# Kernel tuning notes

Hardware: AMD Instinct MI355X
Metric: run time of the kernel (lower is better)

The kernel has to match this reference:

```python
import jax, jax.numpy as jnp
import numpy as np
import math

NH, NKV, HD = 8, 1, 128
SOFTCAP = 30.0
ROPE_BASE = 500000.0


def _rope_tables(T, hd, base):
    half = hd // 2
    inv_freq = 1.0 / (base ** (np.arange(half, dtype=np.float32) / half))
    t = np.arange(T, dtype=np.float32)
    ang = np.outer(t, inv_freq)  # [T, half]
    return jnp.asarray(np.cos(ang)), jnp.asarray(np.sin(ang))


def apply_rope(x, cos, sin):
    # x: [B, T, H, hd]; cos/sin: [T, hd//2]
    half = x.shape[-1] // 2
    x1, x2 = x[..., :half], x[..., half:]
    T = x.shape[1]
    c = cos[:T][None, :, None, :]
    s = sin[:T][None, :, None, :]
    return jnp.concatenate([x1 * c - x2 * s, x1 * s + x2 * c], axis=-1)


def setup_inputs() -> dict:
    key = jax.random.key(0)
    ks = jax.random.split(key, 5)
    B, T, D = 4, 2048, 1024
    KD = NKV * HD
    x = jax.random.normal(ks[0], (B, T, D), dtype=jnp.float32)
    Wq = jax.random.normal(ks[1], (D, D), dtype=jnp.float32) * (D ** -0.5)
    Wk = jax.random.normal(ks[2], (KD, D), dtype=jnp.float32) * (D ** -0.5)
    Wv = jax.random.normal(ks[3], (KD, D), dtype=jnp.float32) * (D ** -0.5)
    Wo = jax.random.normal(ks[4], (D, D), dtype=jnp.float32) * (D ** -0.5)
    qk_gain = jnp.full((NH,), 1.5, dtype=jnp.float32)  # qk_gain_init
    cos, sin = _rope_tables(T, HD, ROPE_BASE)
    return {"x": x, "Wq": Wq, "Wk": Wk, "Wv": Wv, "Wo": Wo,
            "qk_gain": qk_gain, "cos": cos, "sin": sin}


def reference(x, Wq, Wk, Wv, Wo, qk_gain, cos, sin):
    B, T, D = x.shape
    # projections (QuantLinear with qat disabled == plain linear, no bias)
    q = (x @ Wq.T).reshape(B, T, NH, HD)
    k = (x @ Wk.T).reshape(B, T, NKV, HD)
    v = (x @ Wv.T).reshape(B, T, NKV, HD)
    q = apply_rope(q, cos, sin)
    k = apply_rope(k, cos, sin)
    # learned per-head QK gain applied to queries
    q = q * qk_gain[None, None, :, 1 - 1][..., None] if False else q * qk_gain[None, None, :, None]
    # GQA: broadcast the single kv head across NH query heads
    scale = 1.0 / math.sqrt(HD)
    scores = jnp.einsum('bqhd,bkgd->bhqk', q, k) * scale  # g==NKV==1 broadcast
    # logit softcap before masking/softmax
    scores = SOFTCAP * jnp.tanh(scores / SOFTCAP)
    causal = jnp.tril(jnp.ones((T, T), dtype=bool))
    scores = jnp.where(causal[None, None], scores, -jnp.inf)
    attn = jax.nn.softmax(scores, axis=-1)  # [B, NH, T, T]
    out = jnp.einsum('bhqk,bkgd->bqhd', attn, v).reshape(B, T, NH * HD)
    return out @ Wo.T
```

## Files before the change

### kernel.cpp

```cpp
#include <hip/hip_runtime.h>
#include <hip/hip_bf16.h>

#define B_ 4
#define T_ 2048
#define D_ 1024
#define NH_ 8
#define HD_ 128

typedef short short8 __attribute__((ext_vector_type(8)));
typedef float floatx4 __attribute__((ext_vector_type(4)));

#if __has_builtin(__builtin_amdgcn_exp2f)
#define EXP2F __builtin_amdgcn_exp2f
#else
#define EXP2F exp2f
#endif
#if __has_builtin(__builtin_amdgcn_rcpf)
#define RCPF __builtin_amdgcn_rcpf
#else
__device__ __forceinline__ float RCPF(float x) { return 1.f / x; }
#endif

#if __has_builtin(__builtin_amdgcn_global_load_lds)
#define G2L(gp, lp)                                                        \
  __builtin_amdgcn_global_load_lds(                                        \
      (const __attribute__((address_space(1))) unsigned int*)(gp),         \
      (__attribute__((address_space(3))) unsigned int*)(lp), 16, 0, 0)
#else
#define G2L(gp, lp) (*(uint4*)(lp) = *(const uint4*)(gp))
#endif

__device__ __forceinline__ unsigned short f2b(float f) {
  union { float fl; unsigned int i; } v; v.fl = f;
  unsigned int r = v.i + 0x7fffu + ((v.i >> 16) & 1u);
  return (unsigned short)(r >> 16);
}
__device__ __forceinline__ unsigned int pack_bf16(float a, float b) {
  unsigned int ua = __float_as_uint(a) + 0x8000u;
  unsigned int ub = __float_as_uint(b) + 0x8000u;
  return (ua >> 16) | (ub & 0xffff0000u);
}
__device__ __forceinline__ float blo(unsigned int u) { return __uint_as_float(u << 16); }
__device__ __forceinline__ float bhi(unsigned int u) { return __uint_as_float(u & 0xffff0000u); }

__global__ __launch_bounds__(256) void cvt_kernel(
    const float* __restrict__ x,  const float* __restrict__ wq,
    const float* __restrict__ wk, const float* __restrict__ wv,
    const float* __restrict__ wo, unsigned short* __restrict__ dst)
{
  size_t i = ((size_t)blockIdx.x * 256 + threadIdx.x) * 8;
  const float* src; size_t off;
  if      (i <  8388608u) { src = x;  off = i; }
  else if (i <  9437184u) { src = wq; off = i - 8388608u; }
  else if (i <  9568256u) { src = wk; off = i - 9437184u; }
  else if (i <  9699328u) { src = wv; off = i - 9568256u; }
  else                    { src = wo; off = i - 9699328u; }
  float4 a = *(const float4*)(src + off);
  float4 b = *(const float4*)(src + off + 4);
  uint4 o;
  o.x = pack_bf16(a.x, a.y); o.y = pack_bf16(a.z, a.w);
  o.z = pack_bf16(b.x, b.y); o.w = pack_bf16(b.z, b.w);
  *(uint4*)(dst + i) = o;
}

template <bool C_F32>
__device__ __forceinline__ void gemm_body_1024(
    const unsigned short* __restrict__ Arow0,
    const unsigned short* __restrict__ Btile,
    void* __restrict__ Cb, int ldC)
{
  __shared__ unsigned short As[128 * 32];
  __shared__ unsigned short Bs[128 * 32];
  const int tid = threadIdx.x;
  const int lane = tid & 63;
  const int w = tid >> 6;
  const int wr = w >> 1, wc = w & 1;
  const int l15 = lane & 15, quad = lane >> 4;

  const unsigned short* a_src = Arow0 + (size_t)(tid >> 2) * 1024 + (tid & 3) * 8;
  const unsigned short* b_src = Btile + (size_t)(tid >> 2) * 1024 + (tid & 3) * 8;
  unsigned short* a_dst = &As[(tid >> 2) * 32 + (tid & 3) * 8];
  unsigned short* b_dst = &Bs[(tid >> 2) * 32 + (tid & 3) * 8];

  floatx4 zero = {0.f, 0.f, 0.f, 0.f};
  floatx4 acc[4][4];
#pragma unroll
  for (int i = 0; i < 4; i++)
#pragma unroll
    for (int j = 0; j < 4; j++) acc[i][j] = zero;

  for (int k0 = 0; k0 < 1024; k0 += 32) {
    __syncthreads();
    G2L(a_src + k0,         a_dst);
    G2L(a_src + 65536 + k0, a_dst + 2048);
    G2L(b_src + k0,         b_dst);
    G2L(b_src + 65536 + k0, b_dst + 2048);
    __syncthreads();
    short8 af[4], bfr[4];
#pragma unroll
    for (int i = 0; i < 4; i++)
      af[i] = *(const short8*)&As[(wr * 64 + i * 16 + l15) * 32 + quad * 8];
#pragma unroll
    for (int j = 0; j < 4; j++)
      bfr[j] = *(const short8*)&Bs[(wc * 64 + j * 16 + l15) * 32 + quad * 8];
#pragma unroll
    for (int i = 0; i < 4; i++)
#pragma unroll
      for (int j = 0; j < 4; j++)
        acc[i][j] = __builtin_amdgcn_mfma_f32_16x16x32_bf16(af[i], bfr[j], acc[i][j], 0, 0, 0);
  }
#pragma unroll
  for (int i = 0; i < 4; i++)
#pragma unroll
    for (int j = 0; j < 4; j++)
#pragma unroll
      for (int r = 0; r < 4; r++) {
        size_t off = (size_t)(wr * 64 + i * 16 + quad * 4 + r) * ldC + wc * 64 + j * 16 + l15;
        if (C_F32) ((float*)Cb)[off] = acc[i][j][r];
        else ((unsigned short*)Cb)[off] = f2b(acc[i][j][r]);
      }
}

__global__ __launch_bounds__(256) void gemm_qkv_kernel(
    const unsigned short* __restrict__ x,
    const unsigned short* __restrict__ Wq,
    const unsigned short* __restrict__ Wk,
    const unsigned short* __restrict__ Wv,
    unsigned short* __restrict__ q,
    unsigned short* __restrict__ k,
    unsigned short* __restrict__ v)
{
  const int bx = blockIdx.x, by = blockIdx.y;
  const unsigned short* Btile;
  unsigned short* C;
  int ldC, col0;
  if (by < 8) { Btile = Wq + (size_t)by * 128 * 1024; C = q; ldC = 1024; col0 = by * 128; }
  else if (by == 8) { Btile = Wk; C = k; ldC = 128; col0 = 0; }
  else { Btile = Wv; C = v; ldC = 128; col0 = 0; }
  gemm_body_1024<false>(x + (size_t)bx * 128 * 1024, Btile,
                        C + (size_t)bx * 128 * ldC + col0, ldC);
}

__global__ __launch_bounds__(256) void gemm_out_kernel(
    const unsigned short* __restrict__ ao,
    const unsigned short* __restrict__ Wo,
    float* __restrict__ out)
{
  const int bx = blockIdx.x, by = blockIdx.y;
  gemm_body_1024<true>(ao + (size_t)bx * 128 * 1024, Wo + (size_t)by * 128 * 1024,
                       out + (size_t)bx * 128 * 1024 + by * 128, 1024);
}

__global__ __launch_bounds__(256) void rope_kernel(
    unsigned short* __restrict__ q,
    unsigned short* __restrict__ k,
    const float* __restrict__ cosT,
    const float* __restrict__ sinT,
    const float* __restrict__ gain)
{
  const int NQ = B_ * T_ * NH_ * 64;
  int idx = blockIdx.x * 256 + threadIdx.x;
  if (idx < NQ) {
    int i = idx & 63, h = (idx >> 6) & 7, bt = idx >> 9, t = bt & (T_ - 1);
    float c = cosT[t * 64 + i], s = sinT[t * 64 + i];
    float g = gain[h] * 0.0029462782549439484f;
    size_t base = (size_t)bt * 1024 + h * 128;
    float x1 = __bfloat162float(*(const __hip_bfloat16*)&q[base + i]);
    float x2 = __bfloat162float(*(const __hip_bfloat16*)&q[base + 64 + i]);
    q[base + i]      = f2b((x1 * c - x2 * s) * g);
    q[base + 64 + i] = f2b((x1 * s + x2 * c) * g);
  } else if (idx < NQ + B_ * T_ * 64) {
    int j = idx - NQ;
    int i = j & 63, bt = j >> 6, t = bt & (T_ - 1);
    float c = cosT[t * 64 + i], s = sinT[t * 64 + i];
    size_t base = (size_t)bt * 128;
    float x1 = __bfloat162float(*(const __hip_bfloat16*)&k[base + i]);
    float x2 = __bfloat162float(*(const __hip_bfloat16*)&k[base + 64 + i]);
    k[base + i]      = f2b(x1 * c - x2 * s);
    k[base + 64 + i] = f2b(x1 * s + x2 * c);
  }
}

__global__ __launch_bounds__(256) void vtrans_kernel(
    const unsigned short* __restrict__ v,
    unsigned short* __restrict__ vT)
{
  __shared__ unsigned short tile[32 * 136];
  const int b = blockIdx.y, t0 = blockIdx.x * 32, tid = threadIdx.x;
  for (int u = tid; u < 512; u += 256) {
    int r = u >> 4, c = u & 15;
    *(uint4*)&tile[r * 136 + c * 8] =
        *(const uint4*)(v + ((size_t)(b * T_ + t0 + r)) * 128 + c * 8);
  }
  __syncthreads();
  for (int u = tid; u < 512; u += 256) {
    int d = u >> 2, c = u & 3;
    short8 val;
#pragma unroll
    for (int j = 0; j < 8; j++) val[j] = (short)tile[(c * 8 + j) * 136 + d];
    *(short8*)(vT + ((size_t)(b * 128 + d)) * T_ + t0 + c * 8) = val;
  }
}

template <int SPLIT>
__global__ __launch_bounds__(256) void attn_kernel(
    const unsigned short* __restrict__ q,
    const unsigned short* __restrict__ k,
    const unsigned short* __restrict__ vT,
    unsigned short* __restrict__ ao,
    unsigned short* __restrict__ O0,
    float* __restrict__ l0,
    float* __restrict__ l1)
{
  __shared__ unsigned short Ks[16 * 264];
  __shared__ unsigned short Vts[128 * 40];
  __shared__ unsigned short Pw[4][32 * 40];

  const int h = blockIdx.y, b = blockIdx.z;
  const int pr   = SPLIT ? (blockIdx.x >> 1) : blockIdx.x;
  const int half = SPLIT ? (blockIdx.x & 1) : 0;
  const int tid = threadIdx.x, lane = tid & 63, w = tid >> 6;
  const int l15 = lane & 15, quad = lane >> 4;

  const unsigned short* ksrc =
      k + (size_t)b * T_ * 128 + (size_t)(tid >> 4) * 128 + (tid & 15) * 8;
  unsigned short* kdst0 = &Ks[(tid & 15) * 264 + (tid >> 4) * 8];
  unsigned short* kdst1 = kdst0 + 16 * 8;
  const unsigned short* vsrc =
      vT + (size_t)b * 128 * T_ + (size_t)(tid >> 2) * T_ + (tid & 3) * 8;
  unsigned short* vdst0 = &Vts[(tid >> 2) * 40 + (tid & 3) * 8];
  unsigned short* vdst1 = vdst0 + 64 * 40;

  const floatx4 zero = {0.f, 0.f, 0.f, 0.f};

  for (int pass = 0; pass < 2; pass++) {
    const int qblock = pass ? (15 - pr) : pr;
    const int qbase = qblock * 128;
    const int qw = qbase + w * 32;
    int ktBeg, ktEnd;
    if (SPLIT) {
      int hn = 2 * qblock + 2;
      ktBeg = half ? hn : 0;
      ktEnd = half ? 2 * hn : hn;
    } else {
      ktBeg = 0;
      ktEnd = 4 * qblock + 4;
    }

    short8 qf[2][4];
#pragma unroll
    for (int g = 0; g < 2; g++) {
      const unsigned short* qrow =
          q + ((size_t)(b * T_ + qw + g * 16 + l15) * NH_ + h) * HD_;
#pragma unroll
      for (int c = 0; c < 4; c++) qf[g][c] = *(const short8*)(qrow + c * 32 + quad * 8);
    }

    float l_i[2] = {0.f, 0.f};
    floatx4 acc[8][2];
#pragma unroll
    for (int d = 0; d < 8; d++) { acc[d][0] = zero; acc[d][1] = zero; }

    uint4 kr0 = *(const uint4*)(ksrc + (size_t)ktBeg * 4096);
    uint4 kr1 = *(const uint4*)(ksrc + (size_t)ktBeg * 4096 + 2048);
    uint4 vr0 = *(const uint4*)(vsrc + ktBeg * 32);
    uint4 vr1 = *(const uint4*)(vsrc + (size_t)64 * T_ + ktBeg * 32);

    for (int kt = ktBeg; kt < ktEnd; kt++) {
      __syncthreads();
      *(uint4*)kdst0 = kr0; *(uint4*)kdst1 = kr1;
      *(uint4*)vdst0 = vr0; *(uint4*)vdst1 = vr1;
      int ktn = (kt + 1 < ktEnd) ? kt + 1 : kt;
      kr0 = *(const uint4*)(ksrc + (size_t)ktn * 4096);
      kr1 = *(const uint4*)(ksrc + (size_t)ktn * 4096 + 2048);
      vr0 = *(const uint4*)(vsrc + ktn * 32);
      vr1 = *(const uint4*)(vsrc + (size_t)64 * T_ + ktn * 32);
      __syncthreads();

      if (kt * 32 <= qw + 31) {
        floatx4 st[2][2] = {{zero, zero}, {zero, zero}};
#pragma unroll
        for (int c = 0; c < 4; c++) {
          const int dg = (c * 4 + quad) * 264;
          short8 kf0 = *(const short8*)&Ks[dg + l15 * 8];
          short8 kf1 = *(const short8*)&Ks[dg + (16 + l15) * 8];
          st[0][0] = __builtin_amdgcn_mfma_f32_16x16x32_bf16(kf0, qf[0][c], st[0][0], 0, 0, 0);
          st[0][1] = __builtin_amdgcn_mfma_f32_16x16x32_bf16(kf0, qf[1][c], st[0][1], 0, 0, 0);
          st[1][0] = __builtin_amdgcn_mfma_f32_16x16x32_bf16(kf1, qf[0][c], st[1][0], 0, 0, 0);
          st[1][1] = __builtin_amdgcn_mfma_f32_16x16x32_bf16(kf1, qf[1][c], st[1][1], 0, 0, 0);
        }
        float rs[2] = {0.f, 0.f};
#pragma unroll
        for (int f = 0; f < 2; f++)
#pragma unroll
          for (int g = 0; g < 2; g++) {
            float pv[4];
            const int qrow = qw + g * 16 + l15;
#pragma unroll
            for (int r = 0; r < 4; r++) {
              float s = st[f][g][r];
              float e = EXP2F(2.8853901f * s);
              float u = RCPF(e + 1.f);
              float p = EXP2F(-86.561707f * u);
              int key = kt * 32 + f * 16 + quad * 4 + r;
              p = (key <= qrow) ? p : 0.f;
              pv[r] = p;
              rs[g] += p;
            }
            uint2 pk;
            pk.x = pack_bf16(pv[0], pv[1]);
            pk.y = pack_bf16(pv[2], pv[3]);
            *(uint2*)&Pw[w][(g * 16 + l15) * 40 + f * 16 + quad * 4] = pk;
          }
#pragma unroll
        for (int g = 0; g < 2; g++) {
          float r2 = rs[g] + __shfl_xor(rs[g], 16);
          l_i[g] += r2 + __shfl_xor(r2, 32);
        }
        asm volatile("s_waitcnt lgkmcnt(0)" ::: "memory");
        short8 pf0 = *(const short8*)&Pw[w][l15 * 40 + quad * 8];
        short8 pf1 = *(const short8*)&Pw[w][(16 + l15) * 40 + quad * 8];
#pragma unroll
        for (int d = 0; d < 8; d++) {
          short8 vf = *(const short8*)&Vts[(d * 16 + l15) * 40 + quad * 8];
          acc[d][0] = __builtin_amdgcn_mfma_f32_16x16x32_bf16(vf, pf0, acc[d][0], 0, 0, 0);
          acc[d][1] = __builtin_amdgcn_mfma_f32_16x16x32_bf16(vf, pf1, acc[d][1], 0, 0, 0);
        }
      }
    }

#pragma unroll
    for (int g = 0; g < 2; g++) {
      const size_t rowidx = (size_t)(b * T_ + qw + g * 16 + l15) * NH_ + h;
      if (!SPLIT) {
        float linv = 1.f / l_i[g];
        unsigned short* aop = ao + rowidx * HD_ + quad * 4;
#pragma unroll
        for (int d = 0; d < 8; d++) {
          uint2 o;
          o.x = pack_bf16(acc[d][g][0] * linv, acc[d][g][1] * linv);
          o.y = pack_bf16(acc[d][g][2] * linv, acc[d][g][3] * linv);
          *(uint2*)(aop + d * 16) = o;
        }
      } else {
        unsigned short* dst = (half ? ao : O0) + rowidx * HD_ + quad * 4;
#pragma unroll
        for (int d = 0; d < 8; d++) {
          uint2 o;
          o.x = pack_bf16(acc[d][g][0], acc[d][g][1]);
          o.y = pack_bf16(acc[d][g][2], acc[d][g][3]);
          *(uint2*)(dst + d * 16) = o;
        }
        if (quad == 0) (half ? l1 : l0)[rowidx] = l_i[g];
      }
    }
  }
}

__global__ __launch_bounds__(256) void combine_kernel(
    const unsigned short* __restrict__ O0,
    const float* __restrict__ l0,
    const float* __restrict__ l1,
    unsigned short* __restrict__ ao)
{
  size_t i = ((size_t)blockIdx.x * 256 + threadIdx.x) * 8;
  size_t r = i >> 7;
  float linv = RCPF(l0[r] + l1[r]);
  uint4 a = *(const uint4*)(O0 + i);
  uint4 c = *(const uint4*)(ao + i);
  uint4 o;
  o.x = pack_bf16((blo(a.x) + blo(c.x)) * linv, (bhi(a.x) + bhi(c.x)) * linv);
  o.y = pack_bf16((blo(a.y) + blo(c.y)) * linv, (bhi(a.y) + bhi(c.y)) * linv);
  o.z = pack_bf16((blo(a.z) + blo(c.z)) * linv, (bhi(a.z) + bhi(c.z)) * linv);
  o.w = pack_bf16((blo(a.w) + blo(c.w)) * linv, (bhi(a.w) + bhi(c.w)) * linv);
  *(uint4*)(ao + i) = o;
}

extern "C" void kernel_launch(void* const* d_in, const int* in_sizes, int n_in,
                              void* d_out, int out_size, void* d_ws, size_t ws_size,
                              hipStream_t stream) {
  const float* x    = (const float*)d_in[0];
  const float* Wq   = (const float*)d_in[1];
  const float* Wk   = (const float*)d_in[2];
  const float* Wv   = (const float*)d_in[3];
  const float* Wo   = (const float*)d_in[4];
  const float* gain = (const float*)d_in[5];
  const float* cosT = (const float*)d_in[6];
  const float* sinT = (const float*)d_in[7];
  float* out = (float*)d_out;

  unsigned short* ws = (unsigned short*)d_ws;
  unsigned short* blob = ws;
  unsigned short* xb  = blob;
  unsigned short* Wqb = blob + 8388608u;
  unsigned short* Wkb = blob + 9437184u;
  unsigned short* Wvb = blob + 9568256u;
  unsigned short* Wob = blob + 9699328u;
  unsigned short* q   = ws + 10747904u;
  unsigned short* kk  = ws + 19136512u;
  unsigned short* v   = ws + 20185088u;
  unsigned short* vT  = ws + 21233664u;
  unsigned short* ao  = xb;
  unsigned short* O0 = ws + 22282240u;
  float* l0 = (float*)((char*)d_ws + 61341696u);
  float* l1 = (float*)((char*)d_ws + 61603840u);
  const bool split = ws_size >= 61865984ull;

  cvt_kernel<<<5248, 256, 0, stream>>>(x, Wq, Wk, Wv, Wo, blob);
  gemm_qkv_kernel<<<dim3(64, 10), 256, 0, stream>>>(xb, Wqb, Wkb, Wvb, q, kk, v);
  rope_kernel<<<18432, 256, 0, stream>>>(q, kk, cosT, sinT, gain);
  vtrans_kernel<<<dim3(64, 4), 256, 0, stream>>>(v, vT);
  if (split) {
    attn_kernel<1><<<dim3(16, 8, 4), 256, 0, stream>>>(q, kk, vT, ao, O0, l0, l1);
    combine_kernel<<<4096, 256, 0, stream>>>(O0, l0, l1, ao);
  } else {
    attn_kernel<0><<<dim3(8, 8, 4), 256, 0, stream>>>(q, kk, vT, ao, O0, l0, l1);
  }
  gemm_out_kernel<<<dim3(64, 8), 256, 0, stream>>>(ao, Wob, out);
}
```

Measured before the change: 246.3 us.

## Generalize attention KV split to four parts and fuse rope with V transpose

Attention now splits each query block's key range into NSPLIT parts (4 when the workspace is large enough), launching twice as many blocks, and a generalized combine kernel sums the partial outputs and denominators. The rope and V-transpose kernels are merged into one prep launch, and rope now processes 8 elements per thread with vector loads. This aims to raise occupancy across the GPU's compute units during attention and to cut launch and memory-access overhead. In exchange it adds more partial-output traffic in bf16 and a larger workspace requirement.

```diff
diff --git a/kernel.cpp b/kernel.cpp
--- a/kernel.cpp
+++ b/kernel.cpp
@@ -151,74 +151,103 @@
                        out + (size_t)bx * 128 * 1024 + by * 128, 1024);
 }
 
-__global__ __launch_bounds__(256) void rope_kernel(
+__global__ __launch_bounds__(256) void prep_kernel(
     unsigned short* __restrict__ q,
     unsigned short* __restrict__ k,
+    const unsigned short* __restrict__ v,
+    unsigned short* __restrict__ vT,
     const float* __restrict__ cosT,
     const float* __restrict__ sinT,
     const float* __restrict__ gain)
 {
-  const int NQ = B_ * T_ * NH_ * 64;
-  int idx = blockIdx.x * 256 + threadIdx.x;
-  if (idx < NQ) {
-    int i = idx & 63, h = (idx >> 6) & 7, bt = idx >> 9, t = bt & (T_ - 1);
-    float c = cosT[t * 64 + i], s = sinT[t * 64 + i];
-    float g = gain[h] * 0.0029462782549439484f;
-    size_t base = (size_t)bt * 1024 + h * 128;
-    float x1 = __bfloat162float(*(const __hip_bfloat16*)&q[base + i]);
-    float x2 = __bfloat162float(*(const __hip_bfloat16*)&q[base + 64 + i]);
-    q[base + i]      = f2b((x1 * c - x2 * s) * g);
-    q[base + 64 + i] = f2b((x1 * s + x2 * c) * g);
-  } else if (idx < NQ + B_ * T_ * 64) {
-    int j = idx - NQ;
-    int i = j & 63, bt = j >> 6, t = bt & (T_ - 1);
-    float c = cosT[t * 64 + i], s = sinT[t * 64 + i];
-    size_t base = (size_t)bt * 128;
-    float x1 = __bfloat162float(*(const __hip_bfloat16*)&k[base + i]);
-    float x2 = __bfloat162float(*(const __hip_bfloat16*)&k[base + 64 + i]);
-    k[base + i]      = f2b(x1 * c - x2 * s);
-    k[base + 64 + i] = f2b(x1 * s + x2 * c);
-  }
-}
-
-__global__ __launch_bounds__(256) void vtrans_kernel(
-    const unsigned short* __restrict__ v,
-    unsigned short* __restrict__ vT)
-{
   __shared__ unsigned short tile[32 * 136];
-  const int b = blockIdx.y, t0 = blockIdx.x * 32, tid = threadIdx.x;
-  for (int u = tid; u < 512; u += 256) {
-    int r = u >> 4, c = u & 15;
-    *(uint4*)&tile[r * 136 + c * 8] =
-        *(const uint4*)(v + ((size_t)(b * T_ + t0 + r)) * 128 + c * 8);
-  }
-  __syncthreads();
-  for (int u = tid; u < 512; u += 256) {
-    int d = u >> 2, c = u & 3;
-    short8 val;
-#pragma unroll
-    for (int j = 0; j < 8; j++) val[j] = (short)tile[(c * 8 + j) * 136 + d];
-    *(short8*)(vT + ((size_t)(b * 128 + d)) * T_ + t0 + c * 8) = val;
-  }
-}
-
-template <int SPLIT>
+  const int tid = threadIdx.x;
+  if (blockIdx.x < 256) {
+    const int b = blockIdx.x >> 6, t0 = (blockIdx.x & 63) * 32;
+    for (int u = tid; u < 512; u += 256) {
+      int r = u >> 4, c = u & 15;
+      *(uint4*)&tile[r * 136 + c * 8] =
+          *(const uint4*)(v + ((size_t)(b * T_ + t0 + r)) * 128 + c * 8);
+    }
+    __syncthreads();
+    for (int u = tid; u < 512; u += 256) {
+      int d = u >> 2, c = u & 3;
+      short8 val;
+#pragma unroll
+      for (int j = 0; j < 8; j++) val[j] = (short)tile[(c * 8 + j) * 136 + d];
+      *(short8*)(vT + ((size_t)(b * 128 + d)) * T_ + t0 + c * 8) = val;
+    }
+    return;
+  }
+  int idx = (blockIdx.x - 256) * 256 + tid;
+  unsigned short* ptr;
+  size_t base;
+  int t, j;
+  float g;
+  if (idx < 524288) {
+    j = idx & 7;
+    int h = (idx >> 3) & 7;
+    int bt = idx >> 6;
+    t = bt & (T_ - 1);
+    base = (size_t)bt * 1024 + h * 128 + j * 8;
+    ptr = q;
+    g = gain[h] * 0.0029462782549439484f;
+  } else {
+    int id = idx - 524288;
+    j = id & 7;
+    int bt = id >> 3;
+    t = bt & (T_ - 1);
+    base = (size_t)bt * 128 + j * 8;
+    ptr = k;
+    g = 1.f;
+  }
+  float4 ca = *(const float4*)&cosT[t * 64 + j * 8];
+  float4 cb = *(const float4*)&cosT[t * 64 + j * 8 + 4];
+  float4 sa = *(const float4*)&sinT[t * 64 + j * 8];
+  float4 sb = *(const float4*)&sinT[t * 64 + j * 8 + 4];
+  uint4 lo = *(const uint4*)(ptr + base);
+  uint4 hi = *(const uint4*)(ptr + base + 64);
+  uint4 olo, ohi;
+  {
+    float a0 = blo(lo.x), a1 = bhi(lo.x), b0 = blo(hi.x), b1 = bhi(hi.x);
+    olo.x = pack_bf16((a0 * ca.x - b0 * sa.x) * g, (a1 * ca.y - b1 * sa.y) * g);
+    ohi.x = pack_bf16((a0 * sa.x + b0 * ca.x) * g, (a1 * sa.y + b1 * ca.y) * g);
+  }
+  {
+    float a0 = blo(lo.y), a1 = bhi(lo.y), b0 = blo(hi.y), b1 = bhi(hi.y);
+    olo.y = pack_bf16((a0 * ca.z - b0 * sa.z) * g, (a1 * ca.w - b1 * sa.w) * g);
+    ohi.y = pack_bf16((a0 * sa.z + b0 * ca.z) * g, (a1 * sa.w + b1 * ca.w) * g);
+  }
+  {
+    float a0 = blo(lo.z), a1 = bhi(lo.z), b0 = blo(hi.z), b1 = bhi(hi.z);
+    olo.z = pack_bf16((a0 * cb.x - b0 * sb.x) * g, (a1 * cb.y - b1 * sb.y) * g);
+    ohi.z = pack_bf16((a0 * sb.x + b0 * cb.x) * g, (a1 * sb.y + b1 * cb.y) * g);
+  }
+  {
+    float a0 = blo(lo.w), a1 = bhi(lo.w), b0 = blo(hi.w), b1 = bhi(hi.w);
+    olo.w = pack_bf16((a0 * cb.z - b0 * sb.z) * g, (a1 * cb.w - b1 * sb.w) * g);
+    ohi.w = pack_bf16((a0 * sb.z + b0 * cb.z) * g, (a1 * sb.w + b1 * cb.w) * g);
+  }
+  *(uint4*)(ptr + base) = olo;
+  *(uint4*)(ptr + base + 64) = ohi;
+}
+
+template <int NSPLIT>
 __global__ __launch_bounds__(256) void attn_kernel(
     const unsigned short* __restrict__ q,
     const unsigned short* __restrict__ k,
     const unsigned short* __restrict__ vT,
     unsigned short* __restrict__ ao,
-    unsigned short* __restrict__ O0,
-    float* __restrict__ l0,
-    float* __restrict__ l1)
+    unsigned short* __restrict__ Opart,
+    float* __restrict__ lbuf)
 {
   __shared__ unsigned short Ks[16 * 264];
   __shared__ unsigned short Vts[128 * 40];
   __shared__ unsigned short Pw[4][32 * 40];
 
   const int h = blockIdx.y, b = blockIdx.z;
-  const int pr   = SPLIT ? (blockIdx.x >> 1) : blockIdx.x;
-  const int half = SPLIT ? (blockIdx.x & 1) : 0;
+  const int pr   = blockIdx.x / NSPLIT;
+  const int part = blockIdx.x % NSPLIT;
   const int tid = threadIdx.x, lane = tid & 63, w = tid >> 6;
   const int l15 = lane & 15, quad = lane >> 4;
 
@@ -237,15 +266,8 @@
     const int qblock = pass ? (15 - pr) : pr;
     const int qbase = qblock * 128;
     const int qw = qbase + w * 32;
-    int ktBeg, ktEnd;
-    if (SPLIT) {
-      int hn = 2 * qblock + 2;
-      ktBeg = half ? hn : 0;
-      ktEnd = half ? 2 * hn : hn;
-    } else {
-      ktBeg = 0;
-      ktEnd = 4 * qblock + 4;
-    }
+    const int seg = (4 * qblock + 4) / NSPLIT;
+    const int ktBeg = part * seg, ktEnd = ktBeg + seg;
 
     short8 qf[2][4];
 #pragma unroll
@@ -332,7 +354,7 @@
 #pragma unroll
     for (int g = 0; g < 2; g++) {
       const size_t rowidx = (size_t)(b * T_ + qw + g * 16 + l15) * NH_ + h;
-      if (!SPLIT) {
+      if (NSPLIT == 1) {
         float linv = 1.f / l_i[g];
         unsigned short* aop = ao + rowidx * HD_ + quad * 4;
 #pragma unroll
@@ -343,7 +365,9 @@
           *(uint2*)(aop + d * 16) = o;
         }
       } else {
-        unsigned short* dst = (half ? ao : O0) + rowidx * HD_ + quad * 4;
+        unsigned short* dst =
+            ((part == NSPLIT - 1) ? ao : Opart + (size_t)part * 8388608u) +
+            rowidx * HD_ + quad * 4;
 #pragma unroll
         for (int d = 0; d < 8; d++) {
           uint2 o;
@@ -351,28 +375,38 @@
           o.y = pack_bf16(acc[d][g][2], acc[d][g][3]);
           *(uint2*)(dst + d * 16) = o;
         }
-        if (quad == 0) (half ? l1 : l0)[rowidx] = l_i[g];
+        if (quad == 0) lbuf[(size_t)part * 65536u + rowidx] = l_i[g];
       }
     }
   }
 }
 
+template <int NSPLIT>
 __global__ __launch_bounds__(256) void combine_kernel(
-    const unsigned short* __restrict__ O0,
-    const float* __restrict__ l0,
-    const float* __restrict__ l1,
+    const unsigned short* __restrict__ Opart,
+    const float* __restrict__ lbuf,
     unsigned short* __restrict__ ao)
 {
   size_t i = ((size_t)blockIdx.x * 256 + threadIdx.x) * 8;
   size_t r = i >> 7;
-  float linv = RCPF(l0[r] + l1[r]);
-  uint4 a = *(const uint4*)(O0 + i);
+  float ls = 0.f;
+#pragma unroll
+  for (int p = 0; p < NSPLIT; p++) ls += lbuf[(size_t)p * 65536u + r];
+  float linv = RCPF(ls);
   uint4 c = *(const uint4*)(ao + i);
+  float v0 = blo(c.x), v1 = bhi(c.x), v2 = blo(c.y), v3 = bhi(c.y);
+  float v4 = blo(c.z), v5 = bhi(c.z), v6 = blo(c.w), v7 = bhi(c.w);
+#pragma unroll
+  for (int p = 0; p < NSPLIT - 1; p++) {
+    uint4 a = *(const uint4*)(Opart + (size_t)p * 8388608u + i);
+    v0 += blo(a.x); v1 += bhi(a.x); v2 += blo(a.y); v3 += bhi(a.y);
+    v4 += blo(a.z); v5 += bhi(a.z); v6 += blo(a.w); v7 += bhi(a.w);
+  }
   uint4 o;
-  o.x = pack_bf16((blo(a.x) + blo(c.x)) * linv, (bhi(a.x) + bhi(c.x)) * linv);
-  o.y = pack_bf16((blo(a.y) + blo(c.y)) * linv, (bhi(a.y) + bhi(c.y)) * linv);
-  o.z = pack_bf16((blo(a.z) + blo(c.z)) * linv, (bhi(a.z) + bhi(c.z)) * linv);
-  o.w = pack_bf16((blo(a.w) + blo(c.w)) * linv, (bhi(a.w) + bhi(c.w)) * linv);
+  o.x = pack_bf16(v0 * linv, v1 * linv);
+  o.y = pack_bf16(v2 * linv, v3 * linv);
+  o.z = pack_bf16(v4 * linv, v5 * linv);
+  o.w = pack_bf16(v6 * linv, v7 * linv);
   *(uint4*)(ao + i) = o;
 }
 
@@ -401,20 +435,23 @@
   unsigned short* v   = ws + 20185088u;
   unsigned short* vT  = ws + 21233664u;
   unsigned short* ao  = xb;
-  unsigned short* O0 = ws + 22282240u;
-  float* l0 = (float*)((char*)d_ws + 61341696u);
-  float* l1 = (float*)((char*)d_ws + 61603840u);
-  const bool split = ws_size >= 61865984ull;
+  unsigned short* Opart = ws + 22282240u;
+  float* l2 = (float*)((char*)d_ws + 61341696u);
+  float* l4 = (float*)((char*)d_ws + 94896128u);
+  const size_t need2 = 61865984ull;
+  const size_t need4 = 95944704ull;
 
   cvt_kernel<<<5248, 256, 0, stream>>>(x, Wq, Wk, Wv, Wo, blob);
   gemm_qkv_kernel<<<dim3(64, 10), 256, 0, stream>>>(xb, Wqb, Wkb, Wvb, q, kk, v);
-  rope_kernel<<<18432, 256, 0, stream>>>(q, kk, cosT, sinT, gain);
-  vtrans_kernel<<<dim3(64, 4), 256, 0, stream>>>(v, vT);
-  if (split) {
-    attn_kernel<1><<<dim3(16, 8, 4), 256, 0, stream>>>(q, kk, vT, ao, O0, l0, l1);
-    combine_kernel<<<4096, 256, 0, stream>>>(O0, l0, l1, ao);
+  prep_kernel<<<2560, 256, 0, stream>>>(q, kk, v, vT, cosT, sinT, gain);
+  if (ws_size >= need4) {
+    attn_kernel<4><<<dim3(32, 8, 4), 256, 0, stream>>>(q, kk, vT, ao, Opart, l4);
+    combine_kernel<4><<<4096, 256, 0, stream>>>(Opart, l4, ao);
+  } else if (ws_size >= need2) {
+    attn_kernel<2><<<dim3(16, 8, 4), 256, 0, stream>>>(q, kk, vT, ao, Opart, l2);
+    combine_kernel<2><<<4096, 256, 0, stream>>>(Opart, l2, ao);
   } else {
-    attn_kernel<0><<<dim3(8, 8, 4), 256, 0, stream>>>(q, kk, vT, ao, O0, l0, l1);
+    attn_kernel<1><<<dim3(8, 8, 4), 256, 0, stream>>>(q, kk, vT, ao, Opart, l2);
   }
   gemm_out_kernel<<<dim3(64, 8), 256, 0, stream>>>(ao, Wob, out);
 }
```

Measured after the change: 254.5 us. 3.3% more time.
